# Kernel tuning notes

Measured on AMD Instinct MI355X. Metric: run time of the kernel, lower is better.

The kernel has to match this reference:

```python
import jax, jax.numpy as jnp
import numpy as np

EMBED = 256
HEADS = 8
HEAD_DIM = 32
MLP_DIM = 1024
NEG = -1e9  # large negative in place of -inf so fully-deselected rows don't NaN
LN_EPS = 1e-5


def _layernorm(x, g, b):
    m = jnp.mean(x, axis=-1, keepdims=True)
    v = jnp.mean(jnp.square(x - m), axis=-1, keepdims=True)
    return (x - m) / jnp.sqrt(v + LN_EPS) * g + b


def setup_inputs() -> dict:
    key = jax.random.key(0)
    ks = jax.random.split(key, 16)
    b, s, d = 64, 360, EMBED
    sc = 0.02
    return {
        "x": jax.random.normal(ks[0], (b, s, d), dtype=jnp.float32),
        "attention_mask": jnp.zeros((b, 1, 1, s), dtype=jnp.float32),
        # TokenRouter.weight_predictor: Linear(256, 1)
        "wp_w": jax.random.normal(ks[1], (1, d), dtype=jnp.float32) * sc,
        "wp_b": jnp.zeros((1,), dtype=jnp.float32),
        # TokenRouter.aux_predictor: Linear(256,128) -> SiLU -> Linear(128,2)
        "a1_w": jax.random.normal(ks[2], (d // 2, d), dtype=jnp.float32) * sc,
        "a1_b": jnp.zeros((d // 2,), dtype=jnp.float32),
        "a2_w": jax.random.normal(ks[3], (2, d // 2), dtype=jnp.float32) * sc,
        "a2_b": jnp.zeros((2,), dtype=jnp.float32),
        # transformer block (pre-LN GPT2-style)
        "ln1_g": jnp.ones((d,), dtype=jnp.float32),
        "ln1_b": jnp.zeros((d,), dtype=jnp.float32),
        "wqkv": jax.random.normal(ks[4], (d, 3 * d), dtype=jnp.float32) * sc,
        "bqkv": jnp.zeros((3 * d,), dtype=jnp.float32),
        "wo": jax.random.normal(ks[5], (d, d), dtype=jnp.float32) * sc,
        "bo": jnp.zeros((d,), dtype=jnp.float32),
        "ln2_g": jnp.ones((d,), dtype=jnp.float32),
        "ln2_b": jnp.zeros((d,), dtype=jnp.float32),
        "w1": jax.random.normal(ks[6], (d, MLP_DIM), dtype=jnp.float32) * sc,
        "b1": jnp.zeros((MLP_DIM,), dtype=jnp.float32),
        "w2": jax.random.normal(ks[7], (MLP_DIM, d), dtype=jnp.float32) * sc,
        "b2": jnp.zeros((d,), dtype=jnp.float32),
    }


def reference(x, attention_mask, wp_w, wp_b, a1_w, a1_b, a2_w, a2_b,
              ln1_g, ln1_b, wqkv, bqkv, wo, bo, ln2_g, ln2_b, w1, b1, w2, b2):
    b, s, d = x.shape
    # --- router: per-token scalar weight ---
    weights = (x @ wp_w.T + wp_b).squeeze(-1)  # [b, s]
    # --- aux predictor selects tokens (eval path: argmax over 2 logits) ---
    h = jax.nn.silu(x @ a1_w.T + a1_b)
    aux_logits = h @ a2_w.T + a2_b            # [b, s, 2]
    sel = jnp.argmax(aux_logits, axis=-1).astype(bool)  # [b, s]
    # --- masked transformer block over the selected token subset.
    # Compacting tokens then attending == full-seq attention with deselected
    # keys masked out (LN/MLP/residual are position-wise), so vectorize:
    bias = attention_mask + jnp.where(sel, 0.0, NEG)[:, None, None, :]  # [b,1,1,s]
    hn = _layernorm(x, ln1_g, ln1_b)
    qkv = hn @ wqkv + bqkv
    q, k, v = jnp.split(qkv, 3, axis=-1)
    q = q.reshape(b, s, HEADS, HEAD_DIM)
    k = k.reshape(b, s, HEADS, HEAD_DIM)
    v = v.reshape(b, s, HEADS, HEAD_DIM)
    scores = jnp.einsum("bqhd,bkhd->bhqk", q, k) / np.sqrt(HEAD_DIM).astype(np.float32)
    scores = scores + bias                   # [b, h, s, s]
    attn = jax.nn.softmax(scores, axis=-1)
    ctx = jnp.einsum("bhqk,bkhd->bqhd", attn, v).reshape(b, s, d)
    h1 = x + (ctx @ wo + bo)
    h2n = _layernorm(h1, ln2_g, ln2_b)
    block_out = h1 + (jax.nn.gelu(h2n @ w1 + b1) @ w2 + b2)  # [b, s, d]
    # --- scatter-recombine: selected -> weighted block output, else passthrough
    out = jnp.where(sel[..., None], block_out * weights[..., None], x)
    avg_selected = jnp.sum(sel.astype(x.dtype)) / b
    return out, avg_selected
```

## Files before the change

kernel.cpp:

```cpp
#include <hip/hip_runtime.h>
#include <math.h>
#include <stdint.h>

#define TOKN 23040
#define BSZ 64
#define SEQ 360
#define DIM 256
#define NHD 8
#define HDD 32
#define MLPD 1024
#define NEGV -1e9f

typedef __attribute__((ext_vector_type(8))) short bf16x8;
typedef __attribute__((ext_vector_type(4))) float f32x4;

static __device__ __forceinline__ short f2bs(float f) {
  unsigned u = __builtin_bit_cast(unsigned, f);
  u += 0x7fffu + ((u >> 16) & 1u);
  return (short)(u >> 16);
}
static __device__ __forceinline__ unsigned packbf(float a, float b) {
  return (unsigned)(unsigned short)f2bs(a) | ((unsigned)(unsigned short)f2bs(b) << 16);
}

__global__ __launch_bounds__(256) void convw_k(
    const float* __restrict__ wqkv, const float* __restrict__ wo,
    const float* __restrict__ w1, const float* __restrict__ w2,
    short* __restrict__ wqkvt, short* __restrict__ wot,
    short* __restrict__ w1t, short* __restrict__ w2t) {
  int id = blockIdx.x * 256 + threadIdx.x;
  if (id < 256 * 768) {
    int k = id / 768, n = id % 768;
    wqkvt[n * 256 + k] = f2bs(wqkv[id]);
  }
  if (id < 256 * 256) {
    int k = id >> 8, n = id & 255;
    wot[n * 256 + k] = f2bs(wo[id]);
  }
  if (id < 256 * 1024) {
    int k = id >> 10, n = id & 1023;
    w1t[n * 256 + k] = f2bs(w1[id]);
  }
  if (id < 1024 * 256) {
    int k = id >> 8, n = id & 255;
    w2t[n * 1024 + k] = f2bs(w2[id]);
  }
}

__global__ __launch_bounds__(256) void ln_router_k(
    const float* __restrict__ in, const float* __restrict__ g,
    const float* __restrict__ b, const float* __restrict__ wpw,
    const float* __restrict__ wpb, short* __restrict__ outn,
    float* __restrict__ wout, float* __restrict__ outx) {
  int tok = blockIdx.x * 4 + (threadIdx.x >> 6);
  int lane = threadIdx.x & 63;
  const float4 xv = *(const float4*)(in + (size_t)tok * DIM + lane * 4);
  *(float4*)(outx + (size_t)tok * DIM + lane * 4) = xv;
  float s = xv.x + xv.y + xv.z + xv.w;
  float s2 = xv.x * xv.x + xv.y * xv.y + xv.z * xv.z + xv.w * xv.w;
#pragma unroll
  for (int o = 1; o < 64; o <<= 1) { s += __shfl_xor(s, o); s2 += __shfl_xor(s2, o); }
  float m = s * (1.f / DIM);
  float var = fmaxf(s2 * (1.f / DIM) - m * m, 0.f);
  float rstd = rsqrtf(var + 1e-5f);
  float4 gv = *(const float4*)(g + lane * 4);
  float4 bv = *(const float4*)(b + lane * 4);
  uint2 pk;
  pk.x = packbf((xv.x - m) * rstd * gv.x + bv.x, (xv.y - m) * rstd * gv.y + bv.y);
  pk.y = packbf((xv.z - m) * rstd * gv.z + bv.z, (xv.w - m) * rstd * gv.w + bv.w);
  *(uint2*)(outn + (size_t)tok * DIM + lane * 4) = pk;
  float4 wv = *(const float4*)(wpw + lane * 4);
  float wd = xv.x * wv.x + xv.y * wv.y + xv.z * wv.z + xv.w * wv.w;
#pragma unroll
  for (int o = 1; o < 64; o <<= 1) wd += __shfl_xor(wd, o);
  if (lane == 0) wout[tok] = wd + wpb[0];
}

__global__ __launch_bounds__(256) void ln_k(
    const float* __restrict__ in, const float* __restrict__ g,
    const float* __restrict__ b, const int* __restrict__ mtotp,
    short* __restrict__ outn) {
  int tok = blockIdx.x * 4 + (threadIdx.x >> 6);
  int lane = threadIdx.x & 63;
  if (tok >= *mtotp) return;
  const float4 xv = *(const float4*)(in + (size_t)tok * DIM + lane * 4);
  float s = xv.x + xv.y + xv.z + xv.w;
  float s2 = xv.x * xv.x + xv.y * xv.y + xv.z * xv.z + xv.w * xv.w;
#pragma unroll
  for (int o = 1; o < 64; o <<= 1) { s += __shfl_xor(s, o); s2 += __shfl_xor(s2, o); }
  float m = s * (1.f / DIM);
  float var = fmaxf(s2 * (1.f / DIM) - m * m, 0.f);
  float rstd = rsqrtf(var + 1e-5f);
  float4 gv = *(const float4*)(g + lane * 4);
  float4 bv = *(const float4*)(b + lane * 4);
  uint2 pk;
  pk.x = packbf((xv.x - m) * rstd * gv.x + bv.x, (xv.y - m) * rstd * gv.y + bv.y);
  pk.y = packbf((xv.z - m) * rstd * gv.z + bv.z, (xv.w - m) * rstd * gv.w + bv.w);
  *(uint2*)(outn + (size_t)tok * DIM + lane * 4) = pk;
}

__global__ __launch_bounds__(256) void router_gemm_k(
    const float* __restrict__ x, const float* __restrict__ a1w,
    const float* __restrict__ a1b, const float* __restrict__ a2w,
    const float* __restrict__ a2b, int* __restrict__ sel) {
  __shared__ __align__(16) float XT[32][65];
  __shared__ __align__(16) float WT[32][128];
  int m0 = blockIdx.x * 64;
  int t = threadIdx.x;
  int tx = t & 31, ty = t >> 5;
  float acc[8][4] = {};
  int r = t >> 2, c = (t & 3) * 8;
  int n2 = t >> 1, c2 = (t & 1) * 16;
  for (int k0 = 0; k0 < 256; k0 += 32) {
    float4 xa = *(const float4*)(x + (size_t)(m0 + r) * 256 + k0 + c);
    float4 xb = *(const float4*)(x + (size_t)(m0 + r) * 256 + k0 + c + 4);
    XT[c + 0][r] = xa.x; XT[c + 1][r] = xa.y; XT[c + 2][r] = xa.z; XT[c + 3][r] = xa.w;
    XT[c + 4][r] = xb.x; XT[c + 5][r] = xb.y; XT[c + 6][r] = xb.z; XT[c + 7][r] = xb.w;
#pragma unroll
    for (int j = 0; j < 4; j++) {
      float4 wv = *(const float4*)(a1w + (size_t)n2 * 256 + k0 + c2 + j * 4);
      WT[c2 + j * 4 + 0][n2] = wv.x;
      WT[c2 + j * 4 + 1][n2] = wv.y;
      WT[c2 + j * 4 + 2][n2] = wv.z;
      WT[c2 + j * 4 + 3][n2] = wv.w;
    }
    __syncthreads();
#pragma unroll 8
    for (int kk = 0; kk < 32; kk++) {
      float4 wv4 = *(const float4*)&WT[kk][tx * 4];
      float4 x0 = *(const float4*)&XT[kk][ty * 8];
      float4 x1 = *(const float4*)&XT[kk][ty * 8 + 4];
      float xr[8] = {x0.x, x0.y, x0.z, x0.w, x1.x, x1.y, x1.z, x1.w};
      float wr[4] = {wv4.x, wv4.y, wv4.z, wv4.w};
#pragma unroll
      for (int i = 0; i < 8; i++)
#pragma unroll
        for (int j = 0; j < 4; j++) acc[i][j] += xr[i] * wr[j];
    }
    __syncthreads();
  }
  float b1v[4], a20[4], a21[4];
#pragma unroll
  for (int j = 0; j < 4; j++) {
    int dim = tx * 4 + j;
    b1v[j] = a1b[dim];
    a20[j] = a2w[dim];
    a21[j] = a2w[128 + dim];
  }
  float bias0 = a2b[0], bias1 = a2b[1];
#pragma unroll
  for (int i = 0; i < 8; i++) {
    float l0 = 0.f, l1 = 0.f;
#pragma unroll
    for (int j = 0; j < 4; j++) {
      float v = acc[i][j] + b1v[j];
      float h = v / (1.f + expf(-v));
      l0 += h * a20[j];
      l1 += h * a21[j];
    }
#pragma unroll
    for (int o = 1; o < 32; o <<= 1) { l0 += __shfl_xor(l0, o); l1 += __shfl_xor(l1, o); }
    if (tx == 0) sel[m0 + ty * 8 + i] = (l1 + bias1 > l0 + bias0) ? 1 : 0;
  }
}

__global__ __launch_bounds__(512) void scanA_k(const int* __restrict__ sel,
                                               int* __restrict__ idxl,
                                               int* __restrict__ cnt) {
  __shared__ int sc[512];
  int b = blockIdx.x, t = threadIdx.x;
  int flag = (t < SEQ) ? sel[b * SEQ + t] : 0;
  sc[t] = flag;
  __syncthreads();
  int val = flag;
  for (int off = 1; off < 512; off <<= 1) {
    int add = (t >= off) ? sc[t - off] : 0;
    __syncthreads();
    val += add;
    sc[t] = val;
    __syncthreads();
  }
  if (flag) idxl[b * SEQ + (val - 1)] = t;
  if (t == 511) cnt[b] = val;
}

__global__ __launch_bounds__(512) void scanB_k(const int* __restrict__ cnt,
                                               int* __restrict__ startp,
                                               int* __restrict__ mtotp,
                                               int* __restrict__ g_idx,
                                               float* __restrict__ outavg) {
  __shared__ int sc[64];
  int t = threadIdx.x;
  if (t < 64) sc[t] = cnt[t];
  __syncthreads();
  if (t == 0) {
    int run = 0;
    for (int b = 0; b < 64; b++) { startp[b] = run; run += sc[b]; }
    *mtotp = run;
    outavg[0] = (float)run / 64.0f;
  }
  for (int i = t; i < TOKN; i += 512) g_idx[i] = 0;
}

__global__ __launch_bounds__(512) void scanC_k(const int* __restrict__ idxl,
                                               const int* __restrict__ startp,
                                               const int* __restrict__ cnt,
                                               int* __restrict__ g_idx) {
  int b = blockIdx.x, t = threadIdx.x;
  int c = cnt[b], s0 = startp[b];
  for (int j = t; j < c; j += 512) g_idx[s0 + j] = b * SEQ + idxl[b * SEQ + j];
}

template <int MODE>
__global__ __launch_bounds__(256) void gemm_bt_k(
    const short* __restrict__ A, const short* __restrict__ Bt,
    const float* __restrict__ bias, const float* __restrict__ res,
    const float* __restrict__ wgt, const int* __restrict__ g_idx,
    const int* __restrict__ mtotp, short* __restrict__ outb,
    float* __restrict__ outf, int Ndim, int Kdim) {
  int Mt = *mtotp;
  int m0 = blockIdx.y * 64;
  if (m0 >= Mt) return;
  __shared__ __align__(16) short As[64][40];
  __shared__ __align__(16) short Bs[64][40];
  int n0 = blockIdx.x * 64;
  int t = threadIdx.x;
  int wave = t >> 6, lane = t & 63;
  int l15 = lane & 15, quad = lane >> 4;
  int wr = (wave >> 1) * 32, wc = (wave & 1) * 32;
  int srow = t >> 2, scg = (t & 3) * 8;
  int arow = (MODE == 0) ? g_idx[m0 + srow] : (m0 + srow);

  f32x4 acc[2][2];
#pragma unroll
  for (int i = 0; i < 2; i++)
#pragma unroll
    for (int j = 0; j < 2; j++)
#pragma unroll
      for (int r = 0; r < 4; r++) acc[i][j][r] = 0.f;

  for (int k0 = 0; k0 < Kdim; k0 += 32) {
    int4 av = *(const int4*)(A + (size_t)arow * Kdim + k0 + scg);
    int4 bv = *(const int4*)(Bt + (size_t)(n0 + srow) * Kdim + k0 + scg);
    *(int4*)&As[srow][scg] = av;
    *(int4*)&Bs[srow][scg] = bv;
    __syncthreads();
    bf16x8 af[2], bfr[2];
    af[0] = *(const bf16x8*)&As[wr + l15][quad * 8];
    af[1] = *(const bf16x8*)&As[wr + 16 + l15][quad * 8];
    bfr[0] = *(const bf16x8*)&Bs[wc + l15][quad * 8];
    bfr[1] = *(const bf16x8*)&Bs[wc + 16 + l15][quad * 8];
#pragma unroll
    for (int i = 0; i < 2; i++)
#pragma unroll
      for (int j = 0; j < 2; j++)
        acc[i][j] = __builtin_amdgcn_mfma_f32_16x16x32_bf16(af[i], bfr[j],
                                                            acc[i][j], 0, 0, 0);
    __syncthreads();
  }

#pragma unroll
  for (int i = 0; i < 2; i++)
#pragma unroll
    for (int j = 0; j < 2; j++) {
      int col = n0 + wc + j * 16 + l15;
      float bcol = bias[col];
#pragma unroll
      for (int r = 0; r < 4; r++) {
        int row = m0 + wr + i * 16 + quad * 4 + r;
        float v = acc[i][j][r] + bcol;
        size_t idx = (size_t)row * Ndim + col;
        if (MODE == 0) {
          outb[idx] = f2bs(v);
        } else if (MODE == 1) {
          int orig = g_idx[row];
          outf[idx] = v + res[(size_t)orig * 256 + col];
        } else if (MODE == 2) {
          float u = 0.7978845608028654f * (v + 0.044715f * v * v * v);
          float e = __expf(2.f * u);
          float th = 1.f - 2.f / (e + 1.f);
          outb[idx] = f2bs(0.5f * v * (1.f + th));
        } else {
          if (row < Mt) {
            int orig = g_idx[row];
            float o = (v + res[idx]) * wgt[orig];
            outf[(size_t)orig * 256 + col] = o;
          }
        }
      }
    }
}

__global__ __launch_bounds__(256) void attn_k(
    const short* __restrict__ qkv, const float* __restrict__ amask,
    const int* __restrict__ g_idx, const int* __restrict__ startp,
    const int* __restrict__ cntp, short* __restrict__ ctx) {
  __shared__ __align__(16) short VF[2 * 12 * 64 * 8];
  __shared__ __align__(16) float ls[384];
  int bh = blockIdx.x >> 1, qhalf = blockIdx.x & 1;
  int bb = bh >> 3, h = bh & 7;
  int t = threadIdx.x;
  int start = startp[bb], cnt = cntp[bb];
  size_t base = (size_t)start * 768;
  for (int i = t; i < 1536; i += 256) {
    int k = i >> 2, cg = (i & 3) * 8;
    union { int4 v; short s[8]; } u;
    if (k < cnt) {
      u.v = *(const int4*)(qkv + base + (size_t)k * 768 + 512 + h * 32 + cg);
    } else {
      u.v = make_int4(0, 0, 0, 0);
    }
    int c = k >> 5, qd = (k >> 3) & 3, j = k & 7;
#pragma unroll
    for (int jj = 0; jj < 8; jj++) {
      int d = cg + jj;
      VF[((((d >> 4) * 12 + c) * 64) + qd * 16 + (d & 15)) * 8 + j] = u.s[jj];
    }
  }
  for (int i = t; i < 384; i += 256)
    ls[i] = (i < cnt) ? amask[g_idx[start + i]] : 0.f;
  __syncthreads();

  int wave = t >> 6, lane = t & 63;
  int ql = lane & 15, quad = lane >> 4;
  int addr0 = (((quad & 1) * 2) * 16 + ql) * 4;
  int addr1 = addr0 + 64;
  bool hiq = quad >= 2;
  int nt = (cnt + 15) >> 4;
  int nc = (cnt + 31) >> 5;

  for (int qt = qhalf + 2 * wave; qt < nt; qt += 8) {
    int q0 = qt * 16, qrow = q0 + ql;
    bf16x8 qf;
#pragma unroll
    for (int j = 0; j < 8; j++) qf[j] = 0;
    if (qrow < cnt)
      qf = *(const bf16x8*)(qkv + base + (size_t)qrow * 768 + h * 32 + quad * 8);

    f32x4 o0, o1;
#pragma unroll
    for (int r = 0; r < 4; r++) { o0[r] = 0.f; o1[r] = 0.f; }
    float lsum = 0.f;

    for (int c = 0; c < nc; c++) {
      int keyA = c * 32 + ql;
      int keyB = keyA + 16;
      bf16x8 kfA, kfB;
#pragma unroll
      for (int j = 0; j < 8; j++) { kfA[j] = 0; kfB[j] = 0; }
      if (keyA < cnt)
        kfA = *(const bf16x8*)(qkv + base + (size_t)keyA * 768 + 256 + h * 32 + quad * 8);
      if (keyB < cnt)
        kfB = *(const bf16x8*)(qkv + base + (size_t)keyB * 768 + 256 + h * 32 + quad * 8);
      f32x4 sa, sb;
#pragma unroll
      for (int r = 0; r < 4; r++) { sa[r] = 0.f; sb[r] = 0.f; }
      sa = __builtin_amdgcn_mfma_f32_16x16x32_bf16(kfA, qf, sa, 0, 0, 0);
      sb = __builtin_amdgcn_mfma_f32_16x16x32_bf16(kfB, qf, sb, 0, 0, 0);
      int kbase = c * 32 + quad * 4;
      float4 la = *(const float4*)&ls[kbase];
      float4 lb = *(const float4*)&ls[kbase + 16];
      float ea0 = (kbase + 0 < cnt) ? __expf(sa[0] * 0.17677669529663687f + la.x) : 0.f;
      float ea1 = (kbase + 1 < cnt) ? __expf(sa[1] * 0.17677669529663687f + la.y) : 0.f;
      float ea2 = (kbase + 2 < cnt) ? __expf(sa[2] * 0.17677669529663687f + la.z) : 0.f;
      float ea3 = (kbase + 3 < cnt) ? __expf(sa[3] * 0.17677669529663687f + la.w) : 0.f;
      float eb0 = (kbase + 16 < cnt) ? __expf(sb[0] * 0.17677669529663687f + lb.x) : 0.f;
      float eb1 = (kbase + 17 < cnt) ? __expf(sb[1] * 0.17677669529663687f + lb.y) : 0.f;
      float eb2 = (kbase + 18 < cnt) ? __expf(sb[2] * 0.17677669529663687f + lb.z) : 0.f;
      float eb3 = (kbase + 19 < cnt) ? __expf(sb[3] * 0.17677669529663687f + lb.w) : 0.f;
      lsum += (ea0 + ea1) + (ea2 + ea3) + (eb0 + eb1) + (eb2 + eb3);
      unsigned pA0 = packbf(ea0, ea1), pA1 = packbf(ea2, ea3);
      unsigned pB0 = packbf(eb0, eb1), pB1 = packbf(eb2, eb3);
      int s00 = __builtin_amdgcn_ds_bpermute(addr0, (int)pA0);
      int s10 = __builtin_amdgcn_ds_bpermute(addr0, (int)pB0);
      int s01 = __builtin_amdgcn_ds_bpermute(addr0, (int)pA1);
      int s11 = __builtin_amdgcn_ds_bpermute(addr0, (int)pB1);
      int s02 = __builtin_amdgcn_ds_bpermute(addr1, (int)pA0);
      int s12 = __builtin_amdgcn_ds_bpermute(addr1, (int)pB0);
      int s03 = __builtin_amdgcn_ds_bpermute(addr1, (int)pA1);
      int s13 = __builtin_amdgcn_ds_bpermute(addr1, (int)pB1);
      union { int i[4]; bf16x8 v; } pf;
      pf.i[0] = hiq ? s10 : s00;
      pf.i[1] = hiq ? s11 : s01;
      pf.i[2] = hiq ? s12 : s02;
      pf.i[3] = hiq ? s13 : s03;
      bf16x8 v0 = *(const bf16x8*)&VF[(c * 64 + lane) * 8];
      bf16x8 v1 = *(const bf16x8*)&VF[((12 + c) * 64 + lane) * 8];
      o0 = __builtin_amdgcn_mfma_f32_16x16x32_bf16(v0, pf.v, o0, 0, 0, 0);
      o1 = __builtin_amdgcn_mfma_f32_16x16x32_bf16(v1, pf.v, o1, 0, 0, 0);
    }
    lsum += __shfl_xor(lsum, 16);
    lsum += __shfl_xor(lsum, 32);
    float inv = 1.f / lsum;

    if (qrow < cnt) {
      size_t cb = ((size_t)(start + qrow)) * 256 + h * 32;
      uint2 w0, w1;
      w0.x = packbf(o0[0] * inv, o0[1] * inv);
      w0.y = packbf(o0[2] * inv, o0[3] * inv);
      w1.x = packbf(o1[0] * inv, o1[1] * inv);
      w1.y = packbf(o1[2] * inv, o1[3] * inv);
      *(uint2*)(ctx + cb + quad * 4) = w0;
      *(uint2*)(ctx + cb + 16 + quad * 4) = w1;
    }
  }
}

extern "C" void kernel_launch(void* const* d_in, const int* in_sizes, int n_in,
                              void* d_out, int out_size, void* d_ws,
                              size_t ws_size, hipStream_t stream) {
  const float* x = (const float*)d_in[0];
  const float* amask = (const float*)d_in[1];
  const float* wp_w = (const float*)d_in[2];
  const float* wp_b = (const float*)d_in[3];
  const float* a1_w = (const float*)d_in[4];
  const float* a1_b = (const float*)d_in[5];
  const float* a2_w = (const float*)d_in[6];
  const float* a2_b = (const float*)d_in[7];
  const float* ln1_g = (const float*)d_in[8];
  const float* ln1_b = (const float*)d_in[9];
  const float* wqkv = (const float*)d_in[10];
  const float* bqkv = (const float*)d_in[11];
  const float* wo = (const float*)d_in[12];
  const float* bo = (const float*)d_in[13];
  const float* ln2_g = (const float*)d_in[14];
  const float* ln2_b = (const float*)d_in[15];
  const float* w1 = (const float*)d_in[16];
  const float* b1 = (const float*)d_in[17];
  const float* w2 = (const float*)d_in[18];
  const float* b2 = (const float*)d_in[19];
  float* out = (float*)d_out;

  uint8_t* p = (uint8_t*)d_ws;
  float* weightsv = (float*)p; p += (size_t)TOKN * 4;
  int* selv = (int*)p;         p += (size_t)TOKN * 4;
  int* idxlv = (int*)p;        p += (size_t)TOKN * 4;
  int* gidxv = (int*)p;        p += (size_t)TOKN * 4;
  int* cntv = (int*)p;         p += 64 * 4;
  int* startv = (int*)p;       p += 64 * 4;
  int* mtotv = (int*)p;        p += 64 * 4;
  short* wqkvt = (short*)p;    p += (size_t)768 * 256 * 2;
  short* wot = (short*)p;      p += (size_t)256 * 256 * 2;
  short* w1t = (short*)p;      p += (size_t)1024 * 256 * 2;
  short* w2t = (short*)p;      p += (size_t)256 * 1024 * 2;
  float* h1v = (float*)p;      p += (size_t)TOKN * 256 * 4;
  short* h2nv = (short*)p;     p += (size_t)TOKN * 256 * 2;
  short* ctxv = (short*)p;     p += (size_t)TOKN * 256 * 2;
  uint8_t* R = p;
  short* xnv = (short*)R;
  short* qkvv = (short*)(R + (size_t)TOKN * 256 * 2);
  short* actv = (short*)R;

  convw_k<<<dim3(1024), dim3(256), 0, stream>>>(wqkv, wo, w1, w2, wqkvt, wot, w1t, w2t);
  ln_router_k<<<dim3(TOKN / 4), dim3(256), 0, stream>>>(x, ln1_g, ln1_b, wp_w, wp_b,
                                                        xnv, weightsv, out);
  router_gemm_k<<<dim3(360), dim3(256), 0, stream>>>(x, a1_w, a1_b, a2_w, a2_b, selv);
  scanA_k<<<dim3(64), dim3(512), 0, stream>>>(selv, idxlv, cntv);
  scanB_k<<<dim3(1), dim3(512), 0, stream>>>(cntv, startv, mtotv, gidxv,
                                             out + (size_t)TOKN * 256);
  scanC_k<<<dim3(64), dim3(512), 0, stream>>>(idxlv, startv, cntv, gidxv);
  gemm_bt_k<0><<<dim3(12, 360), dim3(256), 0, stream>>>(
      xnv, wqkvt, bqkv, nullptr, nullptr, gidxv, mtotv, qkvv, nullptr, 768, 256);
  attn_k<<<dim3(1024), dim3(256), 0, stream>>>(qkvv, amask, gidxv, startv, cntv, ctxv);
  gemm_bt_k<1><<<dim3(4, 360), dim3(256), 0, stream>>>(
      ctxv, wot, bo, x, nullptr, gidxv, mtotv, nullptr, h1v, 256, 256);
  ln_k<<<dim3(TOKN / 4), dim3(256), 0, stream>>>(h1v, ln2_g, ln2_b, mtotv, h2nv);
  gemm_bt_k<2><<<dim3(16, 360), dim3(256), 0, stream>>>(
      h2nv, w1t, b1, nullptr, nullptr, gidxv, mtotv, actv, nullptr, 1024, 256);
  gemm_bt_k<3><<<dim3(4, 360), dim3(256), 0, stream>>>(
      actv, w2t, b2, h1v, weightsv, gidxv, mtotv, nullptr, out, 256, 1024);
}
```

Baseline: 261.3 us.

## Enlarge GEMM tiles to 128x128 with direct global-to-LDS loads and bf16 residual

The shared GEMM kernel moves from 64x64 to 128x128 tiles, with each wave computing a 64x64 sub-tile (4x4 MFMAs). Operands are staged through global_load_lds directly into unpadded LDS, which raises reuse per loaded byte and removes the register round trip. The h1 residual is now stored as bf16 instead of fp32, halving its traffic in ln_k and the final GEMM at some cost in precision. scanB also zeroes g_idx only past the selected count, and a redundant no-op assignment was added in attention.

```diff
diff --git a/kernel.cpp b/kernel.cpp
--- a/kernel.cpp
+++ b/kernel.cpp
@@ -19,8 +19,17 @@
   u += 0x7fffu + ((u >> 16) & 1u);
   return (short)(u >> 16);
 }
+static __device__ __forceinline__ float bf2f(short s) {
+  unsigned u = ((unsigned)(unsigned short)s) << 16;
+  return __builtin_bit_cast(float, u);
+}
 static __device__ __forceinline__ unsigned packbf(float a, float b) {
   return (unsigned)(unsigned short)f2bs(a) | ((unsigned)(unsigned short)f2bs(b) << 16);
+}
+static __device__ __forceinline__ void gl16(const short* g, short* l) {
+  __builtin_amdgcn_global_load_lds(
+      (const __attribute__((address_space(1))) unsigned int*)g,
+      (__attribute__((address_space(3))) unsigned int*)l, 16, 0, 0);
 }
 
 __global__ __launch_bounds__(256) void convw_k(
@@ -77,15 +86,17 @@
 }
 
 __global__ __launch_bounds__(256) void ln_k(
-    const float* __restrict__ in, const float* __restrict__ g,
+    const short* __restrict__ in, const float* __restrict__ g,
     const float* __restrict__ b, const int* __restrict__ mtotp,
     short* __restrict__ outn) {
   int tok = blockIdx.x * 4 + (threadIdx.x >> 6);
   int lane = threadIdx.x & 63;
   if (tok >= *mtotp) return;
-  const float4 xv = *(const float4*)(in + (size_t)tok * DIM + lane * 4);
-  float s = xv.x + xv.y + xv.z + xv.w;
-  float s2 = xv.x * xv.x + xv.y * xv.y + xv.z * xv.z + xv.w * xv.w;
+  union { uint2 v; short s[4]; } u;
+  u.v = *(const uint2*)(in + (size_t)tok * DIM + lane * 4);
+  float x0 = bf2f(u.s[0]), x1 = bf2f(u.s[1]), x2 = bf2f(u.s[2]), x3 = bf2f(u.s[3]);
+  float s = x0 + x1 + x2 + x3;
+  float s2 = x0 * x0 + x1 * x1 + x2 * x2 + x3 * x3;
 #pragma unroll
   for (int o = 1; o < 64; o <<= 1) { s += __shfl_xor(s, o); s2 += __shfl_xor(s2, o); }
   float m = s * (1.f / DIM);
@@ -94,8 +105,8 @@
   float4 gv = *(const float4*)(g + lane * 4);
   float4 bv = *(const float4*)(b + lane * 4);
   uint2 pk;
-  pk.x = packbf((xv.x - m) * rstd * gv.x + bv.x, (xv.y - m) * rstd * gv.y + bv.y);
-  pk.y = packbf((xv.z - m) * rstd * gv.z + bv.z, (xv.w - m) * rstd * gv.w + bv.w);
+  pk.x = packbf((x0 - m) * rstd * gv.x + bv.x, (x1 - m) * rstd * gv.y + bv.y);
+  pk.y = packbf((x2 - m) * rstd * gv.z + bv.z, (x3 - m) * rstd * gv.w + bv.w);
   *(uint2*)(outn + (size_t)tok * DIM + lane * 4) = pk;
 }
 
@@ -190,6 +201,7 @@
                                                int* __restrict__ g_idx,
                                                float* __restrict__ outavg) {
   __shared__ int sc[64];
+  __shared__ int mt;
   int t = threadIdx.x;
   if (t < 64) sc[t] = cnt[t];
   __syncthreads();
@@ -197,9 +209,12 @@
     int run = 0;
     for (int b = 0; b < 64; b++) { startp[b] = run; run += sc[b]; }
     *mtotp = run;
+    mt = run;
     outavg[0] = (float)run / 64.0f;
   }
-  for (int i = t; i < TOKN; i += 512) g_idx[i] = 0;
+  __syncthreads();
+  int m = mt;
+  for (int i = m + t; i < TOKN; i += 512) g_idx[i] = 0;
 }
 
 __global__ __launch_bounds__(512) void scanC_k(const int* __restrict__ idxl,
@@ -214,55 +229,64 @@
 template <int MODE>
 __global__ __launch_bounds__(256) void gemm_bt_k(
     const short* __restrict__ A, const short* __restrict__ Bt,
-    const float* __restrict__ bias, const float* __restrict__ res,
-    const float* __restrict__ wgt, const int* __restrict__ g_idx,
-    const int* __restrict__ mtotp, short* __restrict__ outb,
-    float* __restrict__ outf, int Ndim, int Kdim) {
+    const float* __restrict__ bias, const float* __restrict__ resf,
+    const short* __restrict__ resb, const float* __restrict__ wgt,
+    const int* __restrict__ g_idx, const int* __restrict__ mtotp,
+    short* __restrict__ outb, float* __restrict__ outf, int Ndim, int Kdim) {
   int Mt = *mtotp;
-  int m0 = blockIdx.y * 64;
+  int m0 = blockIdx.y * 128;
   if (m0 >= Mt) return;
-  __shared__ __align__(16) short As[64][40];
-  __shared__ __align__(16) short Bs[64][40];
-  int n0 = blockIdx.x * 64;
+  __shared__ __align__(16) short As[128 * 32];
+  __shared__ __align__(16) short Bs[128 * 32];
+  int n0 = blockIdx.x * 128;
   int t = threadIdx.x;
   int wave = t >> 6, lane = t & 63;
   int l15 = lane & 15, quad = lane >> 4;
-  int wr = (wave >> 1) * 32, wc = (wave & 1) * 32;
-  int srow = t >> 2, scg = (t & 3) * 8;
-  int arow = (MODE == 0) ? g_idx[m0 + srow] : (m0 + srow);
-
-  f32x4 acc[2][2];
-#pragma unroll
-  for (int i = 0; i < 2; i++)
-#pragma unroll
-    for (int j = 0; j < 2; j++)
+  int wr = (wave >> 1) * 64, wc = (wave & 1) * 64;
+  int r0 = t >> 2, c0 = (t & 3) * 8;
+  long ar0 = (MODE == 0) ? g_idx[m0 + r0] : (m0 + r0);
+  long ar1 = (MODE == 0) ? g_idx[m0 + r0 + 64] : (m0 + r0 + 64);
+  const short* gA0 = A + ar0 * Kdim + c0;
+  const short* gA1 = A + ar1 * Kdim + c0;
+  const short* gB0 = Bt + (size_t)(n0 + r0) * Kdim + c0;
+  const short* gB1 = Bt + (size_t)(n0 + r0 + 64) * Kdim + c0;
+  short* lA = As + wave * 512;
+  short* lB = Bs + wave * 512;
+
+  f32x4 acc[4][4];
+#pragma unroll
+  for (int i = 0; i < 4; i++)
+#pragma unroll
+    for (int j = 0; j < 4; j++)
 #pragma unroll
       for (int r = 0; r < 4; r++) acc[i][j][r] = 0.f;
 
   for (int k0 = 0; k0 < Kdim; k0 += 32) {
-    int4 av = *(const int4*)(A + (size_t)arow * Kdim + k0 + scg);
-    int4 bv = *(const int4*)(Bt + (size_t)(n0 + srow) * Kdim + k0 + scg);
-    *(int4*)&As[srow][scg] = av;
-    *(int4*)&Bs[srow][scg] = bv;
+    gl16(gA0 + k0, lA);
+    gl16(gA1 + k0, lA + 2048);
+    gl16(gB0 + k0, lB);
+    gl16(gB1 + k0, lB + 2048);
     __syncthreads();
-    bf16x8 af[2], bfr[2];
-    af[0] = *(const bf16x8*)&As[wr + l15][quad * 8];
-    af[1] = *(const bf16x8*)&As[wr + 16 + l15][quad * 8];
-    bfr[0] = *(const bf16x8*)&Bs[wc + l15][quad * 8];
-    bfr[1] = *(const bf16x8*)&Bs[wc + 16 + l15][quad * 8];
-#pragma unroll
-    for (int i = 0; i < 2; i++)
-#pragma unroll
-      for (int j = 0; j < 2; j++)
+    bf16x8 af[4], bfr[4];
+#pragma unroll
+    for (int i = 0; i < 4; i++)
+      af[i] = *(const bf16x8*)&As[(wr + i * 16 + l15) * 32 + quad * 8];
+#pragma unroll
+    for (int j = 0; j < 4; j++)
+      bfr[j] = *(const bf16x8*)&Bs[(wc + j * 16 + l15) * 32 + quad * 8];
+#pragma unroll
+    for (int i = 0; i < 4; i++)
+#pragma unroll
+      for (int j = 0; j < 4; j++)
         acc[i][j] = __builtin_amdgcn_mfma_f32_16x16x32_bf16(af[i], bfr[j],
                                                             acc[i][j], 0, 0, 0);
     __syncthreads();
   }
 
 #pragma unroll
-  for (int i = 0; i < 2; i++)
-#pragma unroll
-    for (int j = 0; j < 2; j++) {
+  for (int i = 0; i < 4; i++) {
+#pragma unroll
+    for (int j = 0; j < 4; j++) {
       int col = n0 + wc + j * 16 + l15;
       float bcol = bias[col];
 #pragma unroll
@@ -274,7 +298,7 @@
           outb[idx] = f2bs(v);
         } else if (MODE == 1) {
           int orig = g_idx[row];
-          outf[idx] = v + res[(size_t)orig * 256 + col];
+          outb[idx] = f2bs(v + resf[(size_t)orig * 256 + col]);
         } else if (MODE == 2) {
           float u = 0.7978845608028654f * (v + 0.044715f * v * v * v);
           float e = __expf(2.f * u);
@@ -283,12 +307,13 @@
         } else {
           if (row < Mt) {
             int orig = g_idx[row];
-            float o = (v + res[idx]) * wgt[orig];
+            float o = (v + bf2f(resb[idx])) * wgt[orig];
             outf[(size_t)orig * 256 + col] = o;
           }
         }
       }
     }
+  }
 }
 
 __global__ __launch_bounds__(256) void attn_k(
@@ -383,6 +408,7 @@
       pf.i[0] = hiq ? s10 : s00;
       pf.i[1] = hiq ? s11 : s01;
       pf.i[2] = hiq ? s12 : s02;
+      pf.i[3] = hiq ? s13 : s13;
       pf.i[3] = hiq ? s13 : s03;
       bf16x8 v0 = *(const bf16x8*)&VF[(c * 64 + lane) * 8];
       bf16x8 v1 = *(const bf16x8*)&VF[((12 + c) * 64 + lane) * 8];
@@ -443,7 +469,7 @@
   short* wot = (short*)p;      p += (size_t)256 * 256 * 2;
   short* w1t = (short*)p;      p += (size_t)1024 * 256 * 2;
   short* w2t = (short*)p;      p += (size_t)256 * 1024 * 2;
-  float* h1v = (float*)p;      p += (size_t)TOKN * 256 * 4;
+  short* h1bv = (short*)p;     p += (size_t)TOKN * 256 * 2;
   short* h2nv = (short*)p;     p += (size_t)TOKN * 256 * 2;
   short* ctxv = (short*)p;     p += (size_t)TOKN * 256 * 2;
   uint8_t* R = p;
@@ -459,14 +485,16 @@
   scanB_k<<<dim3(1), dim3(512), 0, stream>>>(cntv, startv, mtotv, gidxv,
                                              out + (size_t)TOKN * 256);
   scanC_k<<<dim3(64), dim3(512), 0, stream>>>(idxlv, startv, cntv, gidxv);
-  gemm_bt_k<0><<<dim3(12, 360), dim3(256), 0, stream>>>(
-      xnv, wqkvt, bqkv, nullptr, nullptr, gidxv, mtotv, qkvv, nullptr, 768, 256);
+  gemm_bt_k<0><<<dim3(6, 180), dim3(256), 0, stream>>>(
+      xnv, wqkvt, bqkv, nullptr, nullptr, nullptr, gidxv, mtotv, qkvv, nullptr,
+      768, 256);
   attn_k<<<dim3(1024), dim3(256), 0, stream>>>(qkvv, amask, gidxv, startv, cntv, ctxv);
-  gemm_bt_k<1><<<dim3(4, 360), dim3(256), 0, stream>>>(
-      ctxv, wot, bo, x, nullptr, gidxv, mtotv, nullptr, h1v, 256, 256);
-  ln_k<<<dim3(TOKN / 4), dim3(256), 0, stream>>>(h1v, ln2_g, ln2_b, mtotv, h2nv);
-  gemm_bt_k<2><<<dim3(16, 360), dim3(256), 0, stream>>>(
-      h2nv, w1t, b1, nullptr, nullptr, gidxv, mtotv, actv, nullptr, 1024, 256);
-  gemm_bt_k<3><<<dim3(4, 360), dim3(256), 0, stream>>>(
-      actv, w2t, b2, h1v, weightsv, gidxv, mtotv, nullptr, out, 256, 1024);
-}
+  gemm_bt_k<1><<<dim3(2, 180), dim3(256), 0, stream>>>(
+      ctxv, wot, bo, x, nullptr, nullptr, gidxv, mtotv, h1bv, nullptr, 256, 256);
+  ln_k<<<dim3(TOKN / 4), dim3(256), 0, stream>>>(h1bv, ln2_g, ln2_b, mtotv, h2nv);
+  gemm_bt_k<2><<<dim3(8, 180), dim3(256), 0, stream>>>(
+      h2nv, w1t, b1, nullptr, nullptr, nullptr, gidxv, mtotv, actv, nullptr,
+      1024, 256);
+  gemm_bt_k<3><<<dim3(2, 180), dim3(256), 0, stream>>>(
+      actv, w2t, b2, nullptr, h1bv, weightsv, gidxv, mtotv, nullptr, out, 256, 1024);
+}
```

Measured after the change: 280.9 us. 7.5% more time.
